# Performance work log

Hardware: AMD Instinct MI355X
Metric: run time of the kernel (lower is better)

Reference implementation:

```python
import jax, jax.numpy as jnp
import numpy as np

NEG_SLOPE = 0.2
N_NODES = 50000


def _gat_layer(x, src, dst, invalid, W, al, ar, b):
    # x: [N, Fin]; src/dst: [E] (self-loops appended); invalid: [E] bool
    N = x.shape[0]
    H, F = al.shape
    z = (x @ W).reshape(N, H, F)                       # [N,H,F]
    el = jnp.sum(z * al[None], axis=-1)                # [N,H]
    er = jnp.sum(z * ar[None], axis=-1)                # [N,H]
    e = el[src] + er[dst]                              # [E,H]
    e = jnp.where(e > 0, e, NEG_SLOPE * e)             # LeakyReLU(0.2)
    e = jnp.where(invalid[:, None], -jnp.inf, e)       # removed self-loop edges
    # edge softmax per destination node (every node has a self-loop -> max finite)
    m = jax.ops.segment_max(e, dst, num_segments=N)    # [N,H]
    ex = jnp.exp(e - m[dst])
    ex = jnp.where(invalid[:, None], 0.0, ex)
    s = jax.ops.segment_sum(ex, dst, num_segments=N)   # [N,H]
    alpha = ex / s[dst]                                # [E,H]
    msg = z[src] * alpha[:, :, None]                   # [E,H,F]
    out = jax.ops.segment_sum(msg, dst, num_segments=N)  # [N,H,F]
    out = out + b.reshape(1, H, F)
    return jax.nn.elu(out)


def _with_self_loops(src, dst):
    N = N_NODES
    loop = jnp.arange(N, dtype=src.dtype)
    invalid = jnp.concatenate([src == dst, jnp.zeros(N, dtype=bool)])
    return jnp.concatenate([src, loop]), jnp.concatenate([dst, loop]), invalid


def setup_inputs() -> dict:
    key = jax.random.key(0)
    ks = jax.random.split(key, 12)
    N, Fin, H0, F0, H1, C = N_NODES, 256, 4, 32, 1, 40
    E = 800000
    sc = lambda k, shp, fan: jax.random.normal(k, shp, jnp.float32) * (1.0 / np.sqrt(fan))
    return {
        "x": jax.random.normal(ks[0], (N, Fin), jnp.float32),
        "src": jax.random.randint(ks[1], (E,), 0, N, jnp.int32),
        "dst": jax.random.randint(ks[2], (E,), 0, N, jnp.int32),
        "W0": sc(ks[3], (Fin, H0 * F0), Fin),
        "al0": sc(ks[4], (H0, F0), F0),
        "ar0": sc(ks[5], (H0, F0), F0),
        "b0": jnp.zeros((H0 * F0,), jnp.float32),
        "W1": sc(ks[6], (H0 * F0, H1 * C), H0 * F0),
        "al1": sc(ks[7], (H1, C), C),
        "ar1": sc(ks[8], (H1, C), C),
        "b1": jnp.zeros((C,), jnp.float32),
    }


def reference(x, src, dst, W0, al0, ar0, b0, W1, al1, ar1, b1):
    s, d, invalid = _with_self_loops(src, dst)
    h = _gat_layer(x, s, d, invalid, W0, al0, ar0, b0)   # [N,4,32]
    h = h.reshape(h.shape[0], -1)                        # flatten(1) -> [N,128]
    h = _gat_layer(h, s, d, invalid, W1, al1, ar1, b1)   # [N,1,40]
    return h.mean(axis=1)                                # mean over heads -> [N,40]
```

## Files before the change

kernel.cpp:

```cpp
#include <hip/hip_runtime.h>
#include <stdint.h>

#define NN 50000
#define EE 800000
#define CAP 48
#define NXCD 8
#define NPX 6250
#define EPB 4096
#define NCHUNK 196
#define GB0 782

typedef __bf16 bf16x8 __attribute__((ext_vector_type(8)));
typedef float  f32x4  __attribute__((ext_vector_type(4)));

__device__ __forceinline__ float bflo(unsigned int w){ union{unsigned int i;float f;}c; c.i=w<<16; return c.f; }
__device__ __forceinline__ float bfhi(unsigned int w){ union{unsigned int i;float f;}c; c.i=w&0xFFFF0000u; return c.f; }
__device__ __forceinline__ bf16x8 bf8_zero(){
  bf16x8 v;
  #pragma unroll
  for (int j=0;j<8;++j) v[j]=(__bf16)0.f;
  return v;
}

__global__ __launch_bounds__(256) void k_prep(const float* __restrict__ W0,
                                              const float* __restrict__ W1,
                                              __bf16* __restrict__ Wg,
                                              __bf16* __restrict__ Wg1,
                                              int* __restrict__ cursor,
                                              int* __restrict__ csrv){
  int tg = blockIdx.x*256 + threadIdx.x;
  if (tg < 4096){
    int k8 = tg >> 7, n = tg & 127;
    bf16x8 v;
    #pragma unroll
    for (int j=0;j<8;++j) v[j] = (__bf16)W0[(k8*8+j)*128 + n];
    *(bf16x8*)(Wg + ((size_t)(k8*128 + n))*8) = v;
  } else if (tg < 4096 + 768){
    int idx = tg - 4096;
    int k16 = idx / 48, n = idx - k16*48;
    bf16x8 v;
    #pragma unroll
    for (int j=0;j<8;++j) v[j] = (n < 40) ? (__bf16)W1[(k16*8+j)*40 + n] : (__bf16)0.f;
    *(bf16x8*)(Wg1 + (size_t)idx*8) = v;
  }
  if (tg < NN){
    cursor[tg] = 1;
    csrv[(size_t)tg*CAP] = tg;
  }
}

__global__ __launch_bounds__(256) void k_gemm0_scatter(const float* __restrict__ x,
    const __bf16* __restrict__ Wg, const float* __restrict__ al0, const float* __restrict__ ar0,
    __bf16* __restrict__ z0b, float* __restrict__ el0, float* __restrict__ er0,
    const int* __restrict__ src, const int* __restrict__ dst,
    int* __restrict__ cursor, int* __restrict__ csrv){
  if (blockIdx.x >= GB0){
    const int xcd = blockIdx.x & 7;
    const int chunk = (blockIdx.x - GB0) >> 3;
    const int lo = xcd*NPX, hi = lo + NPX;
    int e0 = chunk*EPB + threadIdx.x*4;
    #pragma unroll
    for (int it=0; it<EPB/1024; ++it, e0 += 1024){
      if (e0 < EE){
        int4 d4 = *(const int4*)(dst + e0);
        int dv[4] = {d4.x, d4.y, d4.z, d4.w};
        #pragma unroll
        for (int j=0;j<4;++j){
          int d = dv[j];
          if (d >= lo && d < hi){
            int s = src[e0 + j];
            unsigned int inv = (s==d) ? 0x80000000u : 0u;
            int pos = atomicAdd(&cursor[d], 1);
            csrv[(size_t)d*CAP + pos] = (int)((unsigned int)s | inv);
          }
        }
      }
    }
    return;
  }
  const int tid = threadIdx.x;
  const int wv = tid >> 6, ln = tid & 63, q = ln >> 4, mr = ln & 15;
  const int nhalf = wv & 1, mhalf = wv >> 1;
  const int m0w = blockIdx.x*64 + mhalf*32;
  const int n0w = nhalf*64;
  f32x4 acc[2][4];
  #pragma unroll
  for (int mt=0;mt<2;++mt)
    #pragma unroll
    for (int nt=0;nt<4;++nt) acc[mt][nt] = (f32x4){0.f,0.f,0.f,0.f};
  const bool av0 = (m0w + mr) < NN;
  const bool av1 = (m0w + 16 + mr) < NN;
  const float* xr0 = x + (size_t)(m0w + mr)*256;
  const float* xr1 = x + (size_t)(m0w + 16 + mr)*256;
  #pragma unroll
  for (int kc=0;kc<8;++kc){
    int ko = kc*32 + q*8;
    bf16x8 a0 = bf8_zero(), a1 = bf8_zero();
    if (av0){
      float4 p = *(const float4*)(xr0 + ko);
      float4 p2 = *(const float4*)(xr0 + ko + 4);
      a0[0]=(__bf16)p.x; a0[1]=(__bf16)p.y; a0[2]=(__bf16)p.z; a0[3]=(__bf16)p.w;
      a0[4]=(__bf16)p2.x; a0[5]=(__bf16)p2.y; a0[6]=(__bf16)p2.z; a0[7]=(__bf16)p2.w;
    }
    if (av1){
      float4 p = *(const float4*)(xr1 + ko);
      float4 p2 = *(const float4*)(xr1 + ko + 4);
      a1[0]=(__bf16)p.x; a1[1]=(__bf16)p.y; a1[2]=(__bf16)p.z; a1[3]=(__bf16)p.w;
      a1[4]=(__bf16)p2.x; a1[5]=(__bf16)p2.y; a1[6]=(__bf16)p2.z; a1[7]=(__bf16)p2.w;
    }
    const __bf16* wb = Wg + ((size_t)((kc*4+q)*128 + n0w + mr))*8;
    #pragma unroll
    for (int nt=0;nt<4;++nt){
      bf16x8 bf = *(const bf16x8*)(wb + (size_t)nt*16*8);
      acc[0][nt] = __builtin_amdgcn_mfma_f32_16x16x32_bf16(a0, bf, acc[0][nt], 0,0,0);
      acc[1][nt] = __builtin_amdgcn_mfma_f32_16x16x32_bf16(a1, bf, acc[1][nt], 0,0,0);
    }
  }
  float alv[4], arv[4];
  #pragma unroll
  for (int nt=0;nt<4;++nt){ int c = n0w + nt*16 + mr; alv[nt]=al0[c]; arv[nt]=ar0[c]; }
  #pragma unroll
  for (int mt=0;mt<2;++mt){
    #pragma unroll
    for (int r=0;r<4;++r){
      int grow = m0w + mt*16 + q*4 + r;
      if (grow < NN){
        #pragma unroll
        for (int nt=0;nt<4;++nt)
          z0b[(size_t)grow*128 + n0w + nt*16 + mr] = (__bf16)acc[mt][nt][r];
      }
      float pl0 = acc[mt][0][r]*alv[0] + acc[mt][1][r]*alv[1];
      float pr0 = acc[mt][0][r]*arv[0] + acc[mt][1][r]*arv[1];
      float pl1 = acc[mt][2][r]*alv[2] + acc[mt][3][r]*alv[3];
      float pr1 = acc[mt][2][r]*arv[2] + acc[mt][3][r]*arv[3];
      #pragma unroll
      for (int off=1; off<16; off<<=1){
        pl0 += __shfl_xor(pl0, off, 16); pr0 += __shfl_xor(pr0, off, 16);
        pl1 += __shfl_xor(pl1, off, 16); pr1 += __shfl_xor(pr1, off, 16);
      }
      if (mr==0 && grow<NN){
        el0[grow*4 + 2*nhalf]   = pl0; er0[grow*4 + 2*nhalf]   = pr0;
        el0[grow*4 + 2*nhalf+1] = pl1; er0[grow*4 + 2*nhalf+1] = pr1;
      }
    }
  }
}

__global__ __launch_bounds__(256) void k_agg0g1(const unsigned short* __restrict__ z0b,
    const float* __restrict__ el0, const float* __restrict__ er0,
    const int* __restrict__ cursor, const int* __restrict__ csrv,
    const float* __restrict__ b0, const __bf16* __restrict__ Wg1,
    const float* __restrict__ al1, const float* __restrict__ ar1,
    __bf16* __restrict__ z1b, float* __restrict__ el1, float* __restrict__ er1){
  __shared__ __bf16 hsh[16][136];
  unsigned int* hshu = (unsigned int*)&hsh[0][0];
  #pragma unroll
  for (int t = threadIdx.x; t < 12*68; t += 256) hshu[4*68 + t] = 0u;

  int lane = threadIdx.x & 63;
  int wv = threadIdx.x >> 6;
  int i0 = __builtin_amdgcn_readfirstlane(blockIdx.x*4);
  int i = i0 + wv;
  int h1 = lane >> 4;
  int lane2 = lane << 1;
  const float erv = er0[(size_t)i*4 + h1];
  float ax=0.f, ay=0.f, s=0.f;
  int p = i*CAP, pe = p + cursor[i];
  for (; p+8<=pe; p+=8){
    int4 va = *(const int4*)(csrv + p);
    int4 vb = *(const int4*)(csrv + p + 4);
    int v[8] = {va.x,va.y,va.z,va.w,vb.x,vb.y,vb.z,vb.w};
    float el[8];
    #pragma unroll
    for (int j=0;j<8;++j) el[j] = el0[(size_t)(v[j]&0x7FFFFFFF)*4 + h1];
    unsigned int zw[8];
    #pragma unroll
    for (int j=0;j<8;++j)
      zw[j] = *(const unsigned int*)(z0b + (size_t)(v[j]&0x7FFFFFFF)*128 + lane2);
    #pragma unroll
    for (int j=0;j<8;++j){
      float e = el[j] + erv;
      e = fmaxf(e, 0.2f*e);
      float w = (v[j] < 0) ? 0.f : __expf(e);
      s += w; ax = fmaf(w, bflo(zw[j]), ax); ay = fmaf(w, bfhi(zw[j]), ay);
    }
  }
  for (; p+4<=pe; p+=4){
    int4 va = *(const int4*)(csrv + p);
    int v[4] = {va.x,va.y,va.z,va.w};
    float el[4];
    #pragma unroll
    for (int j=0;j<4;++j) el[j] = el0[(size_t)(v[j]&0x7FFFFFFF)*4 + h1];
    unsigned int zw[4];
    #pragma unroll
    for (int j=0;j<4;++j)
      zw[j] = *(const unsigned int*)(z0b + (size_t)(v[j]&0x7FFFFFFF)*128 + lane2);
    #pragma unroll
    for (int j=0;j<4;++j){
      float e = el[j] + erv;
      e = fmaxf(e, 0.2f*e);
      float w = (v[j] < 0) ? 0.f : __expf(e);
      s += w; ax = fmaf(w, bflo(zw[j]), ax); ay = fmaf(w, bfhi(zw[j]), ay);
    }
  }
  for (; p<pe; ++p){
    int v = csrv[p];
    int u = v & 0x7FFFFFFF;
    float e = el0[(size_t)u*4 + h1] + erv;
    e = fmaxf(e, 0.2f*e);
    float w = (v < 0) ? 0.f : __expf(e);
    unsigned int zw = *(const unsigned int*)(z0b + (size_t)u*128 + lane2);
    s += w; ax = fmaf(w, bflo(zw), ax); ay = fmaf(w, bfhi(zw), ay);
  }
  float inv = 1.f/s;
  float ox = ax*inv + b0[lane*2], oy = ay*inv + b0[lane*2+1];
  ox = ox>0.f?ox:__expf(ox)-1.f; oy = oy>0.f?oy:__expf(oy)-1.f;
  union { __bf16 b[2]; unsigned int u; } pk;
  pk.b[0]=(__bf16)ox; pk.b[1]=(__bf16)oy;
  hshu[wv*68 + lane] = pk.u;
  __syncthreads();

  if (wv == 0){
    const int q = lane >> 4, mr = lane & 15;
    f32x4 acc1[3];
    #pragma unroll
    for (int nt=0;nt<3;++nt) acc1[nt] = (f32x4){0.f,0.f,0.f,0.f};
    #pragma unroll
    for (int kc=0;kc<4;++kc){
      bf16x8 af = *(const bf16x8*)&hsh[mr][kc*32 + q*8];
      #pragma unroll
      for (int nt=0;nt<3;++nt){
        bf16x8 bf = *(const bf16x8*)(Wg1 + ((size_t)((kc*4+q)*48 + nt*16+mr))*8);
        acc1[nt] = __builtin_amdgcn_mfma_f32_16x16x32_bf16(af, bf, acc1[nt], 0,0,0);
      }
    }
    float alv[3], arv[3];
    #pragma unroll
    for (int nt=0;nt<3;++nt){
      int c = nt*16+mr;
      alv[nt] = (c<40) ? al1[c] : 0.f;
      arv[nt] = (c<40) ? ar1[c] : 0.f;
    }
    #pragma unroll
    for (int r=0;r<4;++r){
      if (q == 0){
        int grow = i0 + r;
        #pragma unroll
        for (int nt=0;nt<3;++nt){
          int c = nt*16+mr;
          if (c < 40) z1b[(size_t)grow*40 + c] = (__bf16)acc1[nt][r];
        }
      }
      float pl = acc1[0][r]*alv[0] + acc1[1][r]*alv[1] + acc1[2][r]*alv[2];
      float pr = acc1[0][r]*arv[0] + acc1[1][r]*arv[1] + acc1[2][r]*arv[2];
      #pragma unroll
      for (int off=1; off<16; off<<=1){ pl += __shfl_xor(pl, off, 16); pr += __shfl_xor(pr, off, 16); }
      if (q==0 && mr==0){ el1[i0+r]=pl; er1[i0+r]=pr; }
    }
  }
}

__global__ __launch_bounds__(256) void k_agg1(const unsigned short* __restrict__ z1b,
    const float* __restrict__ el1, const float* __restrict__ er1,
    const int* __restrict__ cursor, const int* __restrict__ csrv,
    const float* __restrict__ b1, float* __restrict__ out){
  int lane = threadIdx.x & 63;
  int i = __builtin_amdgcn_readfirstlane(blockIdx.x*4 + (threadIdx.x >> 6));
  int fl = (lane < 20) ? (lane<<1) : 0;
  const float erv = er1[i];
  float ax=0.f, ay=0.f, s=0.f;
  int p = i*CAP, pe = p + cursor[i];
  for (; p+8<=pe; p+=8){
    int4 va = *(const int4*)(csrv + p);
    int4 vb = *(const int4*)(csrv + p + 4);
    int v[8] = {va.x,va.y,va.z,va.w,vb.x,vb.y,vb.z,vb.w};
    float el[8];
    #pragma unroll
    for (int j=0;j<8;++j) el[j] = el1[v[j]&0x7FFFFFFF];
    unsigned int zw[8];
    #pragma unroll
    for (int j=0;j<8;++j)
      zw[j] = *(const unsigned int*)(z1b + (size_t)(v[j]&0x7FFFFFFF)*40 + fl);
    #pragma unroll
    for (int j=0;j<8;++j){
      float e = el[j] + erv;
      e = fmaxf(e, 0.2f*e);
      float w = (v[j] < 0) ? 0.f : __expf(e);
      s += w; ax = fmaf(w, bflo(zw[j]), ax); ay = fmaf(w, bfhi(zw[j]), ay);
    }
  }
  for (; p+4<=pe; p+=4){
    int4 va = *(const int4*)(csrv + p);
    int v[4] = {va.x,va.y,va.z,va.w};
    float el[4];
    #pragma unroll
    for (int j=0;j<4;++j) el[j] = el1[v[j]&0x7FFFFFFF];
    unsigned int zw[4];
    #pragma unroll
    for (int j=0;j<4;++j)
      zw[j] = *(const unsigned int*)(z1b + (size_t)(v[j]&0x7FFFFFFF)*40 + fl);
    #pragma unroll
    for (int j=0;j<4;++j){
      float e = el[j] + erv;
      e = fmaxf(e, 0.2f*e);
      float w = (v[j] < 0) ? 0.f : __expf(e);
      s += w; ax = fmaf(w, bflo(zw[j]), ax); ay = fmaf(w, bfhi(zw[j]), ay);
    }
  }
  for (; p<pe; ++p){
    int v = csrv[p];
    int u = v & 0x7FFFFFFF;
    float e = el1[u] + erv;
    e = fmaxf(e, 0.2f*e);
    float w = (v < 0) ? 0.f : __expf(e);
    unsigned int zw = *(const unsigned int*)(z1b + (size_t)u*40 + fl);
    s += w; ax = fmaf(w, bflo(zw), ax); ay = fmaf(w, bfhi(zw), ay);
  }
  if (lane < 20){
    float inv = 1.f/s;
    float ox = ax*inv + b1[lane*2], oy = ay*inv + b1[lane*2+1];
    ox = ox>0.f?ox:__expf(ox)-1.f; oy = oy>0.f?oy:__expf(oy)-1.f;
    *(float2*)(out + (size_t)i*40 + (lane<<1)) = make_float2(ox, oy);
  }
}

extern "C" void kernel_launch(void* const* d_in, const int* in_sizes, int n_in,
                              void* d_out, int out_size, void* d_ws, size_t ws_size,
                              hipStream_t stream){
  const float* x   = (const float*)d_in[0];
  const int*   src = (const int*)d_in[1];
  const int*   dst = (const int*)d_in[2];
  const float* W0  = (const float*)d_in[3];
  const float* al0 = (const float*)d_in[4];
  const float* ar0 = (const float*)d_in[5];
  const float* b0  = (const float*)d_in[6];
  const float* W1  = (const float*)d_in[7];
  const float* al1 = (const float*)d_in[8];
  const float* ar1 = (const float*)d_in[9];
  const float* b1  = (const float*)d_in[10];
  float* out = (float*)d_out;

  __bf16* z0b = (__bf16*)d_ws;
  __bf16* z1b = z0b + (size_t)NN*128;
  __bf16* Wg  = z1b + (size_t)NN*40;
  __bf16* Wg1 = Wg + 32768;
  float* el0 = (float*)(Wg1 + 6144);
  float* er0 = el0 + (size_t)NN*4;
  float* el1 = er0 + (size_t)NN*4;
  float* er1 = el1 + NN;
  int* cursor = (int*)(er1 + NN);
  int* csrv   = cursor + NN;

  k_prep<<<(NN+255)/256, 256, 0, stream>>>(W0, W1, Wg, Wg1, cursor, csrv);
  k_gemm0_scatter<<<GB0 + NCHUNK*NXCD, 256, 0, stream>>>(x, Wg, al0, ar0, z0b, el0, er0,
                                                         src, dst, cursor, csrv);
  k_agg0g1<<<NN/4, 256, 0, stream>>>((const unsigned short*)z0b, el0, er0, cursor, csrv, b0,
                                     Wg1, al1, ar1, z1b, el1, er1);
  k_agg1 <<<NN/4, 256, 0, stream>>>((const unsigned short*)z1b, el1, er1, cursor, csrv, b1, out);
}
```

Before: 238.7 us.

## Run per-wave layer-1 projection without block sync and pack el1 into z1 rows

The layer-1 projection after layer-0 aggregation now runs in each wave on its own node row, with the other MFMA rows zeroed. This removes the block-wide __syncthreads and the idle waves that used to wait while wave 0 ran the MFMA for all four rows. The z1 buffer is widened to 48 bf16 per node so the el1 attention logit sits in the same row as the features. k_agg1 can then fetch el1 and the features from one cache line per neighbor instead of two scattered loads. In exchange each wave runs MFMAs that are three-quarters wasted, and z1 storage grows.

```diff
diff --git a/kernel.cpp b/kernel.cpp
--- a/kernel.cpp
+++ b/kernel.cpp
@@ -146,21 +146,17 @@
   }
 }
 
-__global__ __launch_bounds__(256) void k_agg0g1(const unsigned short* __restrict__ z0b,
+__global__ __launch_bounds__(256) void k_agg0z1(const unsigned short* __restrict__ z0b,
     const float* __restrict__ el0, const float* __restrict__ er0,
     const int* __restrict__ cursor, const int* __restrict__ csrv,
     const float* __restrict__ b0, const __bf16* __restrict__ Wg1,
     const float* __restrict__ al1, const float* __restrict__ ar1,
-    __bf16* __restrict__ z1b, float* __restrict__ el1, float* __restrict__ er1){
-  __shared__ __bf16 hsh[16][136];
-  unsigned int* hshu = (unsigned int*)&hsh[0][0];
-  #pragma unroll
-  for (int t = threadIdx.x; t < 12*68; t += 256) hshu[4*68 + t] = 0u;
+    __bf16* __restrict__ z1e, float* __restrict__ er1){
+  __shared__ unsigned int hshu[4][68];
 
   int lane = threadIdx.x & 63;
   int wv = threadIdx.x >> 6;
-  int i0 = __builtin_amdgcn_readfirstlane(blockIdx.x*4);
-  int i = i0 + wv;
+  int i = __builtin_amdgcn_readfirstlane(blockIdx.x*4) + wv;
   int h1 = lane >> 4;
   int lane2 = lane << 1;
   const float erv = er0[(size_t)i*4 + h1];
@@ -217,51 +213,52 @@
   ox = ox>0.f?ox:__expf(ox)-1.f; oy = oy>0.f?oy:__expf(oy)-1.f;
   union { __bf16 b[2]; unsigned int u; } pk;
   pk.b[0]=(__bf16)ox; pk.b[1]=(__bf16)oy;
-  hshu[wv*68 + lane] = pk.u;
-  __syncthreads();
-
-  if (wv == 0){
-    const int q = lane >> 4, mr = lane & 15;
-    f32x4 acc1[3];
-    #pragma unroll
-    for (int nt=0;nt<3;++nt) acc1[nt] = (f32x4){0.f,0.f,0.f,0.f};
-    #pragma unroll
-    for (int kc=0;kc<4;++kc){
-      bf16x8 af = *(const bf16x8*)&hsh[mr][kc*32 + q*8];
-      #pragma unroll
-      for (int nt=0;nt<3;++nt){
-        bf16x8 bf = *(const bf16x8*)(Wg1 + ((size_t)((kc*4+q)*48 + nt*16+mr))*8);
-        acc1[nt] = __builtin_amdgcn_mfma_f32_16x16x32_bf16(af, bf, acc1[nt], 0,0,0);
-      }
-    }
-    float alv[3], arv[3];
+
+  hshu[wv][lane] = pk.u;
+  asm volatile("s_waitcnt lgkmcnt(0)" ::: "memory");
+  __builtin_amdgcn_sched_barrier(0);
+
+  const int q = h1, mr = lane & 15;
+  const __bf16* hrow = (const __bf16*)&hshu[wv][0];
+  f32x4 acc1[3];
+  #pragma unroll
+  for (int nt=0;nt<3;++nt) acc1[nt] = (f32x4){0.f,0.f,0.f,0.f};
+  #pragma unroll
+  for (int kc=0;kc<4;++kc){
+    bf16x8 af = *(const bf16x8*)(hrow + kc*32 + q*8);
+    if (mr != 0) af = bf8_zero();
+    #pragma unroll
+    for (int nt=0;nt<3;++nt){
+      bf16x8 bf = *(const bf16x8*)(Wg1 + ((size_t)((kc*4+q)*48 + nt*16+mr))*8);
+      acc1[nt] = __builtin_amdgcn_mfma_f32_16x16x32_bf16(af, bf, acc1[nt], 0,0,0);
+    }
+  }
+  float alv[3], arv[3];
+  #pragma unroll
+  for (int nt=0;nt<3;++nt){
+    int c = nt*16+mr;
+    alv[nt] = (c<40) ? al1[c] : 0.f;
+    arv[nt] = (c<40) ? ar1[c] : 0.f;
+  }
+  float pl = acc1[0][0]*alv[0] + acc1[1][0]*alv[1] + acc1[2][0]*alv[2];
+  float pr = acc1[0][0]*arv[0] + acc1[1][0]*arv[1] + acc1[2][0]*arv[2];
+  #pragma unroll
+  for (int off=1; off<16; off<<=1){ pl += __shfl_xor(pl, off, 16); pr += __shfl_xor(pr, off, 16); }
+  if (q == 0){
     #pragma unroll
     for (int nt=0;nt<3;++nt){
       int c = nt*16+mr;
-      alv[nt] = (c<40) ? al1[c] : 0.f;
-      arv[nt] = (c<40) ? ar1[c] : 0.f;
-    }
-    #pragma unroll
-    for (int r=0;r<4;++r){
-      if (q == 0){
-        int grow = i0 + r;
-        #pragma unroll
-        for (int nt=0;nt<3;++nt){
-          int c = nt*16+mr;
-          if (c < 40) z1b[(size_t)grow*40 + c] = (__bf16)acc1[nt][r];
-        }
-      }
-      float pl = acc1[0][r]*alv[0] + acc1[1][r]*alv[1] + acc1[2][r]*alv[2];
-      float pr = acc1[0][r]*arv[0] + acc1[1][r]*arv[1] + acc1[2][r]*arv[2];
-      #pragma unroll
-      for (int off=1; off<16; off<<=1){ pl += __shfl_xor(pl, off, 16); pr += __shfl_xor(pr, off, 16); }
-      if (q==0 && mr==0){ el1[i0+r]=pl; er1[i0+r]=pr; }
-    }
-  }
-}
-
-__global__ __launch_bounds__(256) void k_agg1(const unsigned short* __restrict__ z1b,
-    const float* __restrict__ el1, const float* __restrict__ er1,
+      if (c < 40) z1e[(size_t)i*48 + c] = (__bf16)acc1[nt][0];
+    }
+    if (mr == 0){
+      *(float*)(z1e + (size_t)i*48 + 40) = pl;
+      er1[i] = pr;
+    }
+  }
+}
+
+__global__ __launch_bounds__(256) void k_agg1(const __bf16* __restrict__ z1e,
+    const float* __restrict__ er1,
     const int* __restrict__ cursor, const int* __restrict__ csrv,
     const float* __restrict__ b1, float* __restrict__ out){
   int lane = threadIdx.x & 63;
@@ -275,12 +272,13 @@
     int4 vb = *(const int4*)(csrv + p + 4);
     int v[8] = {va.x,va.y,va.z,va.w,vb.x,vb.y,vb.z,vb.w};
     float el[8];
-    #pragma unroll
-    for (int j=0;j<8;++j) el[j] = el1[v[j]&0x7FFFFFFF];
     unsigned int zw[8];
     #pragma unroll
-    for (int j=0;j<8;++j)
-      zw[j] = *(const unsigned int*)(z1b + (size_t)(v[j]&0x7FFFFFFF)*40 + fl);
+    for (int j=0;j<8;++j){
+      const __bf16* row = z1e + (size_t)(v[j]&0x7FFFFFFF)*48;
+      el[j] = *(const float*)(row + 40);
+      zw[j] = *(const unsigned int*)(row + fl);
+    }
     #pragma unroll
     for (int j=0;j<8;++j){
       float e = el[j] + erv;
@@ -293,12 +291,13 @@
     int4 va = *(const int4*)(csrv + p);
     int v[4] = {va.x,va.y,va.z,va.w};
     float el[4];
-    #pragma unroll
-    for (int j=0;j<4;++j) el[j] = el1[v[j]&0x7FFFFFFF];
     unsigned int zw[4];
     #pragma unroll
-    for (int j=0;j<4;++j)
-      zw[j] = *(const unsigned int*)(z1b + (size_t)(v[j]&0x7FFFFFFF)*40 + fl);
+    for (int j=0;j<4;++j){
+      const __bf16* row = z1e + (size_t)(v[j]&0x7FFFFFFF)*48;
+      el[j] = *(const float*)(row + 40);
+      zw[j] = *(const unsigned int*)(row + fl);
+    }
     #pragma unroll
     for (int j=0;j<4;++j){
       float e = el[j] + erv;
@@ -310,10 +309,11 @@
   for (; p<pe; ++p){
     int v = csrv[p];
     int u = v & 0x7FFFFFFF;
-    float e = el1[u] + erv;
+    const __bf16* row = z1e + (size_t)u*48;
+    float e = *(const float*)(row + 40) + erv;
     e = fmaxf(e, 0.2f*e);
     float w = (v < 0) ? 0.f : __expf(e);
-    unsigned int zw = *(const unsigned int*)(z1b + (size_t)u*40 + fl);
+    unsigned int zw = *(const unsigned int*)(row + fl);
     s += w; ax = fmaf(w, bflo(zw), ax); ay = fmaf(w, bfhi(zw), ay);
   }
   if (lane < 20){
@@ -341,20 +341,19 @@
   float* out = (float*)d_out;
 
   __bf16* z0b = (__bf16*)d_ws;
-  __bf16* z1b = z0b + (size_t)NN*128;
-  __bf16* Wg  = z1b + (size_t)NN*40;
+  __bf16* z1e = z0b + (size_t)NN*128;
+  __bf16* Wg  = z1e + (size_t)NN*48;
   __bf16* Wg1 = Wg + 32768;
   float* el0 = (float*)(Wg1 + 6144);
   float* er0 = el0 + (size_t)NN*4;
-  float* el1 = er0 + (size_t)NN*4;
-  float* er1 = el1 + NN;
+  float* er1 = er0 + (size_t)NN*4;
   int* cursor = (int*)(er1 + NN);
   int* csrv   = cursor + NN;
 
   k_prep<<<(NN+255)/256, 256, 0, stream>>>(W0, W1, Wg, Wg1, cursor, csrv);
   k_gemm0_scatter<<<GB0 + NCHUNK*NXCD, 256, 0, stream>>>(x, Wg, al0, ar0, z0b, el0, er0,
                                                          src, dst, cursor, csrv);
-  k_agg0g1<<<NN/4, 256, 0, stream>>>((const unsigned short*)z0b, el0, er0, cursor, csrv, b0,
-                                     Wg1, al1, ar1, z1b, el1, er1);
-  k_agg1 <<<NN/4, 256, 0, stream>>>((const unsigned short*)z1b, el1, er1, cursor, csrv, b1, out);
-}
+  k_agg0z1<<<NN/4, 256, 0, stream>>>((const unsigned short*)z0b, el0, er0, cursor, csrv, b0,
+                                     Wg1, al1, ar1, z1e, er1);
+  k_agg1 <<<NN/4, 256, 0, stream>>>(z1e, er1, cursor, csrv, b1, out);
+}
```

New measurement: 252.5 us. +5.8%, slower.
